# Performance work log

Hardware: AMD Instinct MI355X
Metric: run time of the kernel (lower is better)

The kernel has to match this reference:

```python
import jax, jax.numpy as jnp
import numpy as np

FRAME_SIZE = 160
LPC_N = 16
T = 2400  # pcm_chunk_size = 160 * 15
B = 1024

SCALE = 255.0 / 32768.0
SCALE_1 = 32768.0 / 255.0
LOG256 = float(np.log(256.0))


def u2l(u):
    # mu-law (0..255) -> linear
    u = u - 128.0
    s = jnp.sign(u)
    u = jnp.abs(u)
    return s * SCALE_1 * (jnp.exp(u / 128.0 * LOG256) - 1.0)


def l2u(x):
    # linear -> mu-law (0..255)
    s = jnp.sign(x)
    x = jnp.abs(x)
    u = s * (128.0 * jnp.log1p(SCALE * x) / LOG256)
    return jnp.clip(128.0 + u, 0.0, 255.0)


def setup_inputs() -> dict:
    key = jax.random.key(0)
    k1, k2 = jax.random.split(key)
    sig = jax.random.uniform(k1, (B, T, 1), dtype=jnp.float32) * 255.0
    lpc = jax.random.normal(k2, (B, 15, LPC_N), dtype=jnp.float32) * 0.1
    return {"sig": sig, "lpc": lpc}


def reference(sig, lpc):
    # decode mu-law input to linear domain
    xt = u2l(sig)[:, :, 0]                          # (B, T)
    # zero-pad LPC_N samples at the front (history)
    xp = jnp.pad(xt, ((0, 0), (LPC_N, 0)))           # (B, T + LPC_N)
    # 16 shifted views: tap i sees xp[:, LPC_N - i : LPC_N - i + T]
    cX = jnp.stack([xp[:, LPC_N - i:LPC_N - i + T] for i in range(LPC_N)],
                   axis=2)                           # (B, T, LPC_N)
    # repeat per-frame LPC coeffs over the 160 samples of each frame
    lpc_rep = jnp.repeat(lpc, FRAME_SIZE, axis=1)    # (B, T, LPC_N)
    pred = -jnp.sum(lpc_rep * cX, axis=2, keepdims=True)  # (B, T, 1)
    return l2u(pred)
```

## Files before the change

kernel.cpp:

```cpp
#include <hip/hip_runtime.h>
#include <hip/hip_bf16.h>

#define T_LEN 2400
#define LPC_N 16
#define FRAME 160
#define CHUNK 800
#define NGRP  (CHUNK / 4)
#define BLOCK 256

__global__ __launch_bounds__(BLOCK)
void diff_pred_26319559589961_kernel(const float* __restrict__ sig,
                                     const float* __restrict__ lpc,
                                     float* __restrict__ out)
{
    __shared__ float xs[CHUNK + LPC_N];

    const int b   = blockIdx.y;
    const int t0  = blockIdx.x * CHUNK;
    const int tid = threadIdx.x;

    if (tid < (CHUNK + LPC_N) / 4) {
        const int t_in = t0 - LPC_N + 4 * tid;
        float4 r;
        if (t_in >= 0) {
            const float4 v = *(const float4*)(sig + (size_t)b * T_LEN + t_in);
            const float ux = v.x - 128.0f, uy = v.y - 128.0f,
                        uz = v.z - 128.0f, uw = v.w - 128.0f;
            r.x = copysignf((32768.0f/255.0f) * (exp2f(fabsf(ux) * 0.0625f) - 1.0f), ux);
            r.y = copysignf((32768.0f/255.0f) * (exp2f(fabsf(uy) * 0.0625f) - 1.0f), uy);
            r.z = copysignf((32768.0f/255.0f) * (exp2f(fabsf(uz) * 0.0625f) - 1.0f), uz);
            r.w = copysignf((32768.0f/255.0f) * (exp2f(fabsf(uw) * 0.0625f) - 1.0f), uw);
        } else {
            r = make_float4(0.0f, 0.0f, 0.0f, 0.0f);
        }
        *(float4*)(xs + 4 * tid) = r;
    }
    __syncthreads();

    if (tid < NGRP) {
        const int t     = t0 + 4 * tid;
        const int frame = t / FRAME;
        const float4* c = (const float4*)(lpc + ((size_t)b * 15 + frame) * LPC_N);
        const float4 c0 = c[0], c1 = c[1], c2 = c[2], c3 = c[3];

        float r[20];
        *(float4*)(r +  0) = *(const float4*)(xs + 4 * tid +  0);
        *(float4*)(r +  4) = *(const float4*)(xs + 4 * tid +  4);
        *(float4*)(r +  8) = *(const float4*)(xs + 4 * tid +  8);
        *(float4*)(r + 12) = *(const float4*)(xs + 4 * tid + 12);
        *(float4*)(r + 16) = *(const float4*)(xs + 4 * tid + 16);

        const float cf[16] = { c0.x, c0.y, c0.z, c0.w,
                               c1.x, c1.y, c1.z, c1.w,
                               c2.x, c2.y, c2.z, c2.w,
                               c3.x, c3.y, c3.z, c3.w };

        float4 o;
        float* op = &o.x;
        #pragma unroll
        for (int k = 0; k < 4; ++k) {
            float acc = 0.0f;
            #pragma unroll
            for (int i = 0; i < LPC_N; ++i)
                acc += cf[i] * r[16 + k - i];
            const float pred = -acc;
            const float u = copysignf(
                16.0f * __log2f(1.0f + (255.0f/32768.0f) * fabsf(pred)), pred);
            op[k] = fminf(fmaxf(128.0f + u, 0.0f), 255.0f);
        }
        *(float4*)(out + (size_t)b * T_LEN + t) = o;
    }
}

extern "C" void kernel_launch(void* const* d_in, const int* in_sizes, int n_in,
                              void* d_out, int out_size, void* d_ws, size_t ws_size,
                              hipStream_t stream) {
    const float* sig = (const float*)d_in[0];
    const float* lpc = (const float*)d_in[1];
    float* out = (float*)d_out;

    const int B = in_sizes[0] / T_LEN;
    dim3 grid(T_LEN / CHUNK, B);
    diff_pred_26319559589961_kernel<<<grid, BLOCK, 0, stream>>>(sig, lpc, out);
}
```

Baseline: 66.09 us.

## Drop shared-memory staging; each thread loads its own window and emits eight outputs

```diff
diff --git a/kernel.cpp b/kernel.cpp
--- a/kernel.cpp
+++ b/kernel.cpp
@@ -1,75 +1,75 @@
 #include <hip/hip_runtime.h>
-#include <hip/hip_bf16.h>
 
 #define T_LEN 2400
 #define LPC_N 16
 #define FRAME 160
-#define CHUNK 800
-#define NGRP  (CHUNK / 4)
+#define OPT   8
+#define GPROW (T_LEN / OPT)
 #define BLOCK 256
+
+typedef float f4 __attribute__((ext_vector_type(4)));
 
 __global__ __launch_bounds__(BLOCK)
 void diff_pred_26319559589961_kernel(const float* __restrict__ sig,
                                      const float* __restrict__ lpc,
-                                     float* __restrict__ out)
+                                     float* __restrict__ out,
+                                     int total_groups)
 {
-    __shared__ float xs[CHUNK + LPC_N];
+    const int g = blockIdx.x * BLOCK + threadIdx.x;
+    if (g >= total_groups) return;
 
-    const int b   = blockIdx.y;
-    const int t0  = blockIdx.x * CHUNK;
-    const int tid = threadIdx.x;
+    const int b     = g / GPROW;
+    const int gi    = g - b * GPROW;
+    const int t     = gi * OPT;
+    const int frame = gi / (FRAME / OPT);
 
-    if (tid < (CHUNK + LPC_N) / 4) {
-        const int t_in = t0 - LPC_N + 4 * tid;
-        float4 r;
-        if (t_in >= 0) {
-            const float4 v = *(const float4*)(sig + (size_t)b * T_LEN + t_in);
+    const float* srow = sig + (size_t)b * T_LEN;
+
+    float x[LPC_N + OPT];
+    #pragma unroll
+    for (int j = 0; j < (LPC_N + OPT) / 4; ++j) {
+        const int ts = t - LPC_N + 4 * j;
+        float4 r = make_float4(0.0f, 0.0f, 0.0f, 0.0f);
+        if (ts >= 0) {
+            const float4 v = *(const float4*)(srow + ts);
             const float ux = v.x - 128.0f, uy = v.y - 128.0f,
                         uz = v.z - 128.0f, uw = v.w - 128.0f;
             r.x = copysignf((32768.0f/255.0f) * (exp2f(fabsf(ux) * 0.0625f) - 1.0f), ux);
             r.y = copysignf((32768.0f/255.0f) * (exp2f(fabsf(uy) * 0.0625f) - 1.0f), uy);
             r.z = copysignf((32768.0f/255.0f) * (exp2f(fabsf(uz) * 0.0625f) - 1.0f), uz);
             r.w = copysignf((32768.0f/255.0f) * (exp2f(fabsf(uw) * 0.0625f) - 1.0f), uw);
-        } else {
-            r = make_float4(0.0f, 0.0f, 0.0f, 0.0f);
         }
-        *(float4*)(xs + 4 * tid) = r;
+        x[4 * j + 0] = r.x;
+        x[4 * j + 1] = r.y;
+        x[4 * j + 2] = r.z;
+        x[4 * j + 3] = r.w;
     }
-    __syncthreads();
 
-    if (tid < NGRP) {
-        const int t     = t0 + 4 * tid;
-        const int frame = t / FRAME;
-        const float4* c = (const float4*)(lpc + ((size_t)b * 15 + frame) * LPC_N);
-        const float4 c0 = c[0], c1 = c[1], c2 = c[2], c3 = c[3];
+    const float4* c = (const float4*)(lpc + ((size_t)b * 15 + frame) * LPC_N);
+    const float4 c0 = c[0], c1 = c[1], c2 = c[2], c3 = c[3];
+    const float cf[16] = { c0.x, c0.y, c0.z, c0.w,
+                           c1.x, c1.y, c1.z, c1.w,
+                           c2.x, c2.y, c2.z, c2.w,
+                           c3.x, c3.y, c3.z, c3.w };
 
-        float r[20];
-        *(float4*)(r +  0) = *(const float4*)(xs + 4 * tid +  0);
-        *(float4*)(r +  4) = *(const float4*)(xs + 4 * tid +  4);
-        *(float4*)(r +  8) = *(const float4*)(xs + 4 * tid +  8);
-        *(float4*)(r + 12) = *(const float4*)(xs + 4 * tid + 12);
-        *(float4*)(r + 16) = *(const float4*)(xs + 4 * tid + 16);
+    float o[OPT];
+    #pragma unroll
+    for (int k = 0; k < OPT; ++k) {
+        float acc = 0.0f;
+        #pragma unroll
+        for (int i = 0; i < LPC_N; ++i)
+            acc += cf[i] * x[LPC_N + k - i];
+        const float pred = -acc;
+        const float u = copysignf(
+            16.0f * __log2f(1.0f + (255.0f/32768.0f) * fabsf(pred)), pred);
+        o[k] = fminf(fmaxf(128.0f + u, 0.0f), 255.0f);
+    }
 
-        const float cf[16] = { c0.x, c0.y, c0.z, c0.w,
-                               c1.x, c1.y, c1.z, c1.w,
-                               c2.x, c2.y, c2.z, c2.w,
-                               c3.x, c3.y, c3.z, c3.w };
-
-        float4 o;
-        float* op = &o.x;
-        #pragma unroll
-        for (int k = 0; k < 4; ++k) {
-            float acc = 0.0f;
-            #pragma unroll
-            for (int i = 0; i < LPC_N; ++i)
-                acc += cf[i] * r[16 + k - i];
-            const float pred = -acc;
-            const float u = copysignf(
-                16.0f * __log2f(1.0f + (255.0f/32768.0f) * fabsf(pred)), pred);
-            op[k] = fminf(fmaxf(128.0f + u, 0.0f), 255.0f);
-        }
-        *(float4*)(out + (size_t)b * T_LEN + t) = o;
-    }
+    float* dst = out + (size_t)b * T_LEN + t;
+    f4 o0 = { o[0], o[1], o[2], o[3] };
+    f4 o1 = { o[4], o[5], o[6], o[7] };
+    __builtin_nontemporal_store(o0, (f4*)dst);
+    __builtin_nontemporal_store(o1, (f4*)(dst + 4));
 }
 
 extern "C" void kernel_launch(void* const* d_in, const int* in_sizes, int n_in,
@@ -80,6 +80,8 @@
     float* out = (float*)d_out;
 
     const int B = in_sizes[0] / T_LEN;
-    dim3 grid(T_LEN / CHUNK, B);
-    diff_pred_26319559589961_kernel<<<grid, BLOCK, 0, stream>>>(sig, lpc, out);
+    const int total_groups = B * GPROW;
+    const int nblk = (total_groups + BLOCK - 1) / BLOCK;
+    diff_pred_26319559589961_kernel<<<dim3(nblk), dim3(BLOCK), 0, stream>>>(
+        sig, lpc, out, total_groups);
 }
```

Result: no change. 66.34 us (+0.4%).
